# Kernel optimization log

Hardware: AMD Instinct MI355X
Metric: run time of the kernel (lower is better)

## Reference

```python
import jax, jax.numpy as jnp
import numpy as np

DIM = 768
HEADS = 12
HEAD_DIM = DIM // HEADS
HIDDEN = int(DIM * 1.0)  # mlp_ratio = 1.0
EPS = 1e-5


def layer_norm(x, g, b):
    mu = jnp.mean(x, axis=-1, keepdims=True)
    var = jnp.mean(jnp.square(x - mu), axis=-1, keepdims=True)
    return (x - mu) * jax.lax.rsqrt(var + EPS) * g + b


def setup_inputs() -> dict:
    key = jax.random.key(0)
    ks = jax.random.split(key, 8)
    s = 0.02
    return {
        "x": jax.random.normal(ks[0], (8, 1024, DIM), dtype=jnp.float32),
        "mask": jnp.ones((8, 1024), dtype=jnp.int32),
        "g1": jnp.ones((DIM,), jnp.float32),
        "b1": jnp.zeros((DIM,), jnp.float32),
        "w_qkv": jax.random.normal(ks[1], (DIM, 3 * DIM), jnp.float32) * s,
        "w_proj": jax.random.normal(ks[2], (DIM, DIM), jnp.float32) * s,
        "b_proj": jnp.zeros((DIM,), jnp.float32),
        "g2": jnp.ones((DIM,), jnp.float32),
        "b2": jnp.zeros((DIM,), jnp.float32),
        "w_fc1": jax.random.normal(ks[3], (DIM, HIDDEN), jnp.float32) * s,
        "b_fc1": jnp.zeros((HIDDEN,), jnp.float32),
        "w_fc2": jax.random.normal(ks[4], (HIDDEN, DIM), jnp.float32) * s,
        "b_fc2": jnp.zeros((DIM,), jnp.float32),
    }


def reference(x, mask, g1, b1, w_qkv, w_proj, b_proj, g2, b2, w_fc1, b_fc1, w_fc2, b_fc2):
    B, N, C = x.shape
    scale = HEAD_DIM ** -0.5

    # --- attention (pre-norm) ---
    h = layer_norm(x, g1, b1)
    qkv = (h @ w_qkv).reshape(B, N, 3, HEADS, HEAD_DIM)
    qkv = jnp.transpose(qkv, (2, 0, 3, 1, 4))  # 3, b, h, n, d
    q, k, v = qkv[0], qkv[1], qkv[2]

    attn = jnp.einsum("bhnd,bhmd->bhnm", q, k) * scale
    # mask: (B, N) -> pairwise mask (B, 1, N, N)
    pair = (mask[:, None, :, None] * mask[:, None, None, :]) != 0
    attn = jnp.where(pair, attn, jnp.float32(-1e9))
    attn = jax.nn.softmax(attn, axis=-1)

    o = jnp.einsum("bhnm,bhmd->bhnd", attn, v)
    o = jnp.transpose(o, (0, 2, 1, 3)).reshape(B, N, C)
    o = o @ w_proj + b_proj
    x = x + o

    # --- MLP (pre-norm) ---
    h2 = layer_norm(x, g2, b2)
    h2 = jax.nn.gelu(h2 @ w_fc1 + b_fc1, approximate=False)
    h2 = h2 @ w_fc2 + b_fc2
    return x + h2
```

## Files before the change

### kernel.cpp

```cpp
#include <hip/hip_runtime.h>
#include <stdint.h>
#include <math.h>

using short8 = __attribute__((ext_vector_type(8))) short;
using f32x4  = __attribute__((ext_vector_type(4))) float;

#define DEV __device__ __forceinline__
#define S_VMCNT(n) asm volatile("s_waitcnt vmcnt(" #n ")" ::: "memory")
#define S_LGKM(n)  asm volatile("s_waitcnt lgkmcnt(" #n ")" ::: "memory")
#define S_LGKM0()  asm volatile("s_waitcnt lgkmcnt(0)" ::: "memory")
#define SCHED0()   __builtin_amdgcn_sched_barrier(0)
#define SBAR()     __builtin_amdgcn_s_barrier()

DEV unsigned short f2bf(float f) {
    union { float f; unsigned u; } c; c.f = f;
    unsigned u = c.u;
    unsigned r = (u + 0x7FFFu + ((u >> 16) & 1u)) >> 16;
    return (unsigned short)r;
}

DEV float bf2f(unsigned short h) {
    union { unsigned u; float f; } c; c.u = ((unsigned)h) << 16;
    return c.f;
}

DEV void gld16(const unsigned short* g, unsigned short* l) {
    __builtin_amdgcn_global_load_lds(
        (const __attribute__((address_space(1))) void*)g,
        (__attribute__((address_space(3))) void*)l, 16, 0, 0);
}

DEV unsigned ldsaddr(unsigned short* p) {
    return (unsigned)(uintptr_t)(__attribute__((address_space(3))) unsigned short*)p;
}

DEV unsigned cvtpk(float lo, float hi) {
    unsigned r;
    asm("v_cvt_pk_bf16_f32 %0, %1, %2" : "=v"(r) : "v"(lo), "v"(hi));
    return r;
}

DEV uint2 tr16(unsigned addr) {
    uint2 r;
    asm volatile("ds_read_b64_tr_b16 %0, %1" : "=v"(r) : "v"(addr));
    return r;
}

__global__ __launch_bounds__(256) void k_transpose_all(
    const float* __restrict__ w0, const float* __restrict__ w1,
    const float* __restrict__ w2, const float* __restrict__ w3,
    unsigned short* __restrict__ o0, unsigned short* __restrict__ o1,
    unsigned short* __restrict__ o2, unsigned short* __restrict__ o3)
{
    __shared__ float tile[32][33];
    int z = blockIdx.z;
    const float* W = (z == 0) ? w0 : (z == 1) ? w1 : (z == 2) ? w2 : w3;
    unsigned short* Wt = (z == 0) ? o0 : (z == 1) ? o1 : (z == 2) ? o2 : o3;
    int N = (z == 0) ? 2304 : 768;
    int n0 = blockIdx.x * 32, k0 = blockIdx.y * 32;
    if (n0 >= N) return;
    int tx = threadIdx.x, ty = threadIdx.y;
#pragma unroll
    for (int i = 0; i < 4; i++) {
        int k = k0 + ty + i * 8;
        tile[ty + i * 8][tx] = W[(size_t)k * N + n0 + tx];
    }
    __syncthreads();
#pragma unroll
    for (int i = 0; i < 4; i++) {
        int n = n0 + ty + i * 8;
        Wt[(size_t)n * 768 + k0 + tx] = f2bf(tile[tx][ty + i * 8]);
    }
}

template<int BF>
__global__ __launch_bounds__(256) void k_layernorm(
    const void* __restrict__ xin, const float* __restrict__ g,
    const float* __restrict__ b, unsigned short* __restrict__ out)
{
    int row = blockIdx.x;
    int tid = threadIdx.x;
    float v0, v1, v2;
    if (BF) {
        const unsigned short* xr = (const unsigned short*)xin + (size_t)row * 768;
        v0 = bf2f(xr[tid]); v1 = bf2f(xr[tid + 256]); v2 = bf2f(xr[tid + 512]);
    } else {
        const float* xr = (const float*)xin + (size_t)row * 768;
        v0 = xr[tid]; v1 = xr[tid + 256]; v2 = xr[tid + 512];
    }
    float s1 = v0 + v1 + v2;
    float s2 = v0 * v0 + v1 * v1 + v2 * v2;
#pragma unroll
    for (int off = 32; off >= 1; off >>= 1) {
        s1 += __shfl_down(s1, off);
        s2 += __shfl_down(s2, off);
    }
    __shared__ float red[8];
    int wid = tid >> 6, lane = tid & 63;
    if (lane == 0) { red[wid] = s1; red[4 + wid] = s2; }
    __syncthreads();
    s1 = red[0] + red[1] + red[2] + red[3];
    s2 = red[4] + red[5] + red[6] + red[7];
    float mu = s1 * (1.0f / 768.0f);
    float var = s2 * (1.0f / 768.0f) - mu * mu;
    float rs = rsqrtf(var + 1e-5f);
    unsigned short* orow = out + (size_t)row * 768;
    orow[tid]       = f2bf((v0 - mu) * rs * g[tid]       + b[tid]);
    orow[tid + 256] = f2bf((v1 - mu) * rs * g[tid + 256] + b[tid + 256]);
    orow[tid + 512] = f2bf((v2 - mu) * rs * g[tid + 512] + b[tid + 512]);
}

template<int EPI, int BN>
__global__ __launch_bounds__(BN == 128 ? 512 : 256) void k_gemm(
    const unsigned short* __restrict__ A, const unsigned short* __restrict__ Bt,
    const float* __restrict__ bias,
    const float* __restrict__ residF, const unsigned short* __restrict__ residH,
    float* __restrict__ outF, unsigned short* __restrict__ outH,
    unsigned short* __restrict__ qb, unsigned short* __restrict__ kb,
    unsigned short* __restrict__ vtb)
{
    constexpr int KK = 768, NK = 12;
    constexpr int MI = 2;
    constexpr int NJ = 4;
    __shared__ __align__(16) unsigned short As[2][128 * 64];
    __shared__ __align__(16) unsigned short Bs[2][BN * 64];

    int tid = threadIdx.x;
    int lane = tid & 63, wid = tid >> 6;

    int gy = gridDim.y;
    int nwg = 64 * gy;
    int bid = blockIdx.x + blockIdx.y * 64;
    int nid = (bid & 7) * (nwg >> 3) + (bid >> 3);
    int bx = nid / gy;
    int by = nid - bx * gy;
    int m0 = bx * 128, n0 = by * BN;

    int wr = (BN == 128) ? (wid >> 1) * 32 : wid * 32;
    int wc = (BN == 128) ? (wid & 1) * 64 : 0;
    int fr = lane & 15, fg = lane >> 4;
    int fr7 = fr & 7;

    f32x4 zero4 = {0.f, 0.f, 0.f, 0.f};
    f32x4 acc[MI][NJ];
#pragma unroll
    for (int mi = 0; mi < MI; mi++)
#pragma unroll
        for (int nj = 0; nj < NJ; nj++) acc[mi][nj] = zero4;

    int srow = tid >> 3;
    int schk = (tid & 7) ^ ((tid >> 3) & 7);
    const unsigned short* ga = A  + (size_t)(m0 + srow) * KK + schk * 8;
    const unsigned short* gb = Bt + (size_t)(n0 + srow) * KK + schk * 8;

    auto stage = [&](int kt, int s) {
        int ko = kt * 64;
        if constexpr (BN == 128) {
            gld16(ga + ko, As[s] + wid * 512);
            gld16(ga + (size_t)64 * KK + ko, As[s] + 4096 + wid * 512);
            gld16(gb + ko, Bs[s] + wid * 512);
            gld16(gb + (size_t)64 * KK + ko, Bs[s] + 4096 + wid * 512);
        } else {
#pragma unroll
            for (int i = 0; i < 4; i++)
                gld16(ga + (size_t)i * 32 * KK + ko, As[s] + i * 2048 + wid * 512);
#pragma unroll
            for (int i = 0; i < 2; i++)
                gld16(gb + (size_t)i * 32 * KK + ko, Bs[s] + i * 2048 + wid * 512);
        }
    };

    int aoff0 = (wr + fr) * 64;
    int boff0 = (wc + fr) * 64;

    stage(0, 0);

    for (int k = 0; k < NK; ++k) {
        if (k + 1 < NK) {
            stage(k + 1, (k + 1) & 1);
            if constexpr (BN == 128) { S_VMCNT(4); } else { S_VMCNT(6); }
        } else {
            S_VMCNT(0);
        }
        SCHED0(); SBAR(); SCHED0();

        const unsigned short* Ac = As[k & 1];
        const unsigned short* Bc = Bs[k & 1];
#pragma unroll
        for (int kk = 0; kk < 2; ++kk) {
            int off = (((kk << 2) | fg) ^ fr7) * 8;
            short8 af[MI], bfv[NJ];
#pragma unroll
            for (int mi = 0; mi < MI; mi++)
                af[mi] = *(const short8*)(Ac + aoff0 + mi * 1024 + off);
#pragma unroll
            for (int nj = 0; nj < NJ; nj++)
                bfv[nj] = *(const short8*)(Bc + boff0 + nj * 1024 + off);
#pragma unroll
            for (int mi = 0; mi < MI; mi++)
#pragma unroll
                for (int nj = 0; nj < NJ; nj++)
                    acc[mi][nj] = __builtin_amdgcn_mfma_f32_16x16x32_bf16(
                        af[mi], bfv[nj], acc[mi][nj], 0, 0, 0);
        }
        SCHED0(); SBAR(); SCHED0();
    }

#pragma unroll
    for (int mi = 0; mi < MI; mi++) {
#pragma unroll
        for (int nj = 0; nj < NJ; nj++) {
#pragma unroll
            for (int i = 0; i < 4; i++) {
                int grow = m0 + wr + mi * 16 + fg * 4 + i;
                int gcol = n0 + wc + nj * 16 + fr;
                float v = acc[mi][nj][i];
                if (EPI == 0) {
                    int part = gcol / 768;
                    int wi = gcol - part * 768;
                    int head = wi >> 6, d = wi & 63;
                    int bb = grow >> 10, n = grow & 1023;
                    size_t base = ((size_t)(bb * 12 + head)) << 16;
                    unsigned short bv = f2bf(v);
                    if (part == 0)      qb[base + (size_t)n * 64 + d] = bv;
                    else if (part == 1) kb[base + (size_t)n * 64 + d] = bv;
                    else                vtb[base + (size_t)d * 1024 + n] = bv;
                } else if (EPI == 1) {
                    size_t idx = (size_t)grow * 768 + gcol;
                    outH[idx] = f2bf(v + bias[gcol] + residF[idx]);
                } else if (EPI == 2) {
                    float t = v + bias[gcol];
                    outH[(size_t)grow * 768 + gcol] =
                        f2bf(0.5f * t * (1.0f + erff(t * 0.70710678118f)));
                } else {
                    size_t idx = (size_t)grow * 768 + gcol;
                    outF[idx] = v + bias[gcol] + bf2f(residH[idx]);
                }
            }
        }
    }
}

__global__ __launch_bounds__(512) void k_attn(
    const unsigned short* __restrict__ Q, const unsigned short* __restrict__ Kk,
    const unsigned short* __restrict__ Vt, const int* __restrict__ mask,
    unsigned short* __restrict__ O)
{
    __shared__ __align__(16) unsigned short KsA[3 * 4096];
    __shared__ __align__(16) unsigned short VsA[3 * 4096];
    __shared__ __align__(16) unsigned short PT[8 * 1024];
    __shared__ float mskf[1024];

    int tid = threadIdx.x, lane = tid & 63, wid = tid >> 6;
    int bid = blockIdx.x + blockIdx.y * 8;
    int nid = (bid & 7) * 96 + (bid >> 3);
    int qt = nid & 7;
    int bh = nid >> 3;
    int b = bh / 12;
    int hh = bh - b * 12;
    int fr = lane & 15, fg = lane >> 4;

    const unsigned short* qg = Q  + ((size_t)bh << 16);
    const unsigned short* kg = Kk + ((size_t)bh << 16);
    const unsigned short* vg = Vt + ((size_t)bh << 16);

    for (int i = tid; i < 1024; i += 512)
        mskf[i] = mask[b * 1024 + i] ? 1.f : 0.f;

    short8 qf[2];
    {
        const unsigned short* qp = qg + (size_t)(qt * 128 + wid * 16 + fr) * 64 + fg * 8;
        qf[0] = *(const short8*)(qp);
        qf[1] = *(const short8*)(qp + 32);
    }

    int srow = wid * 8 + (lane >> 3);
    int schk = (lane & 7) ^ ((lane >> 3) & 7);
    const unsigned short* kgp = kg + (size_t)srow * 64 + schk * 8;
    const unsigned short* vgp = vg + (size_t)srow * 1024 + schk * 8;

    auto stage = [&](int kn, int s) {
        gld16(kgp + (size_t)(kn * 64) * 64, &KsA[s * 4096] + wid * 512);
        gld16(vgp + kn * 64, &VsA[s * 4096] + wid * 512);
    };

    stage(0, 0);
    __syncthreads();

    f32x4 zero4 = {0.f, 0.f, 0.f, 0.f};
    f32x4 oacc[4];
    f32x4 lacc = zero4;
#pragma unroll
    for (int df = 0; df < 4; df++) oacc[df] = zero4;

    short8 ones8;
#pragma unroll
    for (int j = 0; j < 8; j++) ones8[j] = (short)0x3F80;

    const float SC = 0.125f * 1.44269504f;

    unsigned short* pw = &PT[wid * 1024];
    unsigned trbase = ldsaddr(pw) + fg * 256 + fr * 2;

    int pos0 = fg ^ (fr & 7);
    int pos1 = (fg + 4) ^ (fr & 7);

#pragma unroll
    for (int kc = 0; kc < 16; ++kc) {
        S_VMCNT(0);
        SCHED0(); SBAR(); SCHED0();
        if (kc < 15) { stage(kc + 1, (kc + 1) % 3); SCHED0(); }

        const unsigned short* Kc = &KsA[(kc % 3) * 4096];
        short8 kb0[4], kb1[4];
#pragma unroll
        for (int nf = 0; nf < 4; ++nf) {
            int row = nf * 16 + fr;
            kb0[nf] = *(const short8*)(Kc + row * 64 + pos0 * 8);
            kb1[nf] = *(const short8*)(Kc + row * 64 + pos1 * 8);
        }
        SCHED0();

        f32x4 s[4];
        if (kc > 0) {
            S_LGKM(8);
            uint2 r00 = tr16(trbase);
            uint2 r01 = tr16(trbase + 128);
            uint2 r10 = tr16(trbase + 1024);
            uint2 r11 = tr16(trbase + 1024 + 128);
            S_LGKM(4);
            SCHED0();
            __builtin_amdgcn_s_setprio(1);
#pragma unroll
            for (int nf = 0; nf < 4; ++nf) {
                f32x4 a = zero4;
                a = __builtin_amdgcn_mfma_f32_16x16x32_bf16(qf[0], kb0[nf], a, 0, 0, 0);
                a = __builtin_amdgcn_mfma_f32_16x16x32_bf16(qf[1], kb1[nf], a, 0, 0, 0);
                s[nf] = a;
            }
            __builtin_amdgcn_s_setprio(0);

            const unsigned short* Vp = &VsA[(((kc - 1) % 3)) * 4096];
            short8 vb0[4], vb1[4];
#pragma unroll
            for (int df = 0; df < 4; ++df) {
                int rv = df * 16 + fr;
                vb0[df] = *(const short8*)(Vp + rv * 64 + pos0 * 8);
                vb1[df] = *(const short8*)(Vp + rv * 64 + pos1 * 8);
            }

            union { unsigned u[4]; short8 s8; } pa0, pa1;
            pa0.u[0] = r00.x; pa0.u[1] = r00.y; pa0.u[2] = r01.x; pa0.u[3] = r01.y;
            pa1.u[0] = r10.x; pa1.u[1] = r10.y; pa1.u[2] = r11.x; pa1.u[3] = r11.y;

            uint2 w[4];
#pragma unroll
            for (int nf = 0; nf < 4; nf++) {
                float mk = mskf[kc * 64 + nf * 16 + fr];
                float p0 = __builtin_amdgcn_exp2f(s[nf][0] * SC) * mk;
                float p1 = __builtin_amdgcn_exp2f(s[nf][1] * SC) * mk;
                float p2 = __builtin_amdgcn_exp2f(s[nf][2] * SC) * mk;
                float p3 = __builtin_amdgcn_exp2f(s[nf][3] * SC) * mk;
                w[nf].x = cvtpk(p0, p1); w[nf].y = cvtpk(p2, p3);
            }

            S_LGKM0();
            SCHED0();
            __builtin_amdgcn_s_setprio(1);
#pragma unroll
            for (int df = 0; df < 4; df++) {
                oacc[df] = __builtin_amdgcn_mfma_f32_16x16x32_bf16(pa0.s8, vb0[df], oacc[df], 0, 0, 0);
                oacc[df] = __builtin_amdgcn_mfma_f32_16x16x32_bf16(pa1.s8, vb1[df], oacc[df], 0, 0, 0);
            }
            lacc = __builtin_amdgcn_mfma_f32_16x16x32_bf16(pa0.s8, ones8, lacc, 0, 0, 0);
            lacc = __builtin_amdgcn_mfma_f32_16x16x32_bf16(pa1.s8, ones8, lacc, 0, 0, 0);
            __builtin_amdgcn_s_setprio(0);

#pragma unroll
            for (int nf = 0; nf < 4; nf++)
                *(uint2*)(pw + (nf * 16 + fr) * 16 + fg * 4) = w[nf];
        } else {
            S_LGKM0();
            SCHED0();
            __builtin_amdgcn_s_setprio(1);
#pragma unroll
            for (int nf = 0; nf < 4; ++nf) {
                f32x4 a = zero4;
                a = __builtin_amdgcn_mfma_f32_16x16x32_bf16(qf[0], kb0[nf], a, 0, 0, 0);
                a = __builtin_amdgcn_mfma_f32_16x16x32_bf16(qf[1], kb1[nf], a, 0, 0, 0);
                s[nf] = a;
            }
            __builtin_amdgcn_s_setprio(0);
#pragma unroll
            for (int nf = 0; nf < 4; nf++) {
                float mk = mskf[nf * 16 + fr];
                float p0 = __builtin_amdgcn_exp2f(s[nf][0] * SC) * mk;
                float p1 = __builtin_amdgcn_exp2f(s[nf][1] * SC) * mk;
                float p2 = __builtin_amdgcn_exp2f(s[nf][2] * SC) * mk;
                float p3 = __builtin_amdgcn_exp2f(s[nf][3] * SC) * mk;
                uint2 w0; w0.x = cvtpk(p0, p1); w0.y = cvtpk(p2, p3);
                *(uint2*)(pw + (nf * 16 + fr) * 16 + fg * 4) = w0;
            }
        }
    }

    {
        uint2 r00 = tr16(trbase);
        uint2 r01 = tr16(trbase + 128);
        uint2 r10 = tr16(trbase + 1024);
        uint2 r11 = tr16(trbase + 1024 + 128);
        const unsigned short* Vp = &VsA[0];
        short8 vb0[4], vb1[4];
#pragma unroll
        for (int df = 0; df < 4; ++df) {
            int rv = df * 16 + fr;
            vb0[df] = *(const short8*)(Vp + rv * 64 + pos0 * 8);
            vb1[df] = *(const short8*)(Vp + rv * 64 + pos1 * 8);
        }
        S_LGKM0(); SCHED0();
        union { unsigned u[4]; short8 s8; } pa0, pa1;
        pa0.u[0] = r00.x; pa0.u[1] = r00.y; pa0.u[2] = r01.x; pa0.u[3] = r01.y;
        pa1.u[0] = r10.x; pa1.u[1] = r10.y; pa1.u[2] = r11.x; pa1.u[3] = r11.y;
#pragma unroll
        for (int df = 0; df < 4; df++) {
            oacc[df] = __builtin_amdgcn_mfma_f32_16x16x32_bf16(pa0.s8, vb0[df], oacc[df], 0, 0, 0);
            oacc[df] = __builtin_amdgcn_mfma_f32_16x16x32_bf16(pa1.s8, vb1[df], oacc[df], 0, 0, 0);
        }
        lacc = __builtin_amdgcn_mfma_f32_16x16x32_bf16(pa0.s8, ones8, lacc, 0, 0, 0);
        lacc = __builtin_amdgcn_mfma_f32_16x16x32_bf16(pa1.s8, ones8, lacc, 0, 0, 0);
    }

#pragma unroll
    for (int i = 0; i < 4; i++) {
        float inv = 1.0f / fmaxf(lacc[i], 1e-30f);
        size_t rowbase = ((size_t)(b * 1024 + qt * 128 + wid * 16 + fg * 4 + i)) * 768
                         + hh * 64 + fr;
#pragma unroll
        for (int df = 0; df < 4; df++)
            O[rowbase + df * 16] = f2bf(oacc[df][i] * inv);
    }
}

extern "C" void kernel_launch(void* const* d_in, const int* in_sizes, int n_in,
                              void* d_out, int out_size, void* d_ws, size_t ws_size,
                              hipStream_t stream)
{
    const float* x      = (const float*)d_in[0];
    const int*   mask   = (const int*)d_in[1];
    const float* g1     = (const float*)d_in[2];
    const float* b1     = (const float*)d_in[3];
    const float* w_qkv  = (const float*)d_in[4];
    const float* w_proj = (const float*)d_in[5];
    const float* b_proj = (const float*)d_in[6];
    const float* g2     = (const float*)d_in[7];
    const float* b2     = (const float*)d_in[8];
    const float* w_fc1  = (const float*)d_in[9];
    const float* b_fc1  = (const float*)d_in[10];
    const float* w_fc2  = (const float*)d_in[11];
    const float* b_fc2  = (const float*)d_in[12];
    float* out = (float*)d_out;

    char* ws = (char*)d_ws;
    unsigned short* wqkv_t  = (unsigned short*)(ws + 0);
    unsigned short* wproj_t = (unsigned short*)(ws + 3538944);
    unsigned short* wfc1_t  = (unsigned short*)(ws + 4718592);
    unsigned short* wfc2_t  = (unsigned short*)(ws + 5898240);
    unsigned short* bufA    = (unsigned short*)(ws + 7077888);
    unsigned short* bufB    = (unsigned short*)(ws + 19660800);
    unsigned short* qb      = (unsigned short*)(ws + 32243712);
    unsigned short* kb      = (unsigned short*)(ws + 44826624);
    unsigned short* vtb     = (unsigned short*)(ws + 57409536);
    unsigned short* x1b     = (unsigned short*)(ws + 69992448);

    k_transpose_all<<<dim3(72, 24, 4), dim3(32, 8), 0, stream>>>(
        w_qkv, w_proj, w_fc1, w_fc2, wqkv_t, wproj_t, wfc1_t, wfc2_t);

    k_layernorm<0><<<8192, 256, 0, stream>>>(x, g1, b1, bufA);

    k_gemm<0, 128><<<dim3(64, 18), 512, 0, stream>>>(bufA, wqkv_t,
        nullptr, nullptr, nullptr, nullptr, nullptr, qb, kb, vtb);

    k_attn<<<dim3(8, 96), 512, 0, stream>>>(qb, kb, vtb, mask, bufB);

    k_gemm<1, 64><<<dim3(64, 12), 256, 0, stream>>>(bufB, wproj_t,
        b_proj, x, nullptr, nullptr, x1b, nullptr, nullptr, nullptr);

    k_layernorm<1><<<8192, 256, 0, stream>>>(x1b, g2, b2, bufA);

    k_gemm<2, 64><<<dim3(64, 12), 256, 0, stream>>>(bufA, wfc1_t,
        b_fc1, nullptr, nullptr, nullptr, bufB, nullptr, nullptr, nullptr);

    k_gemm<3, 64><<<dim3(64, 12), 256, 0, stream>>>(bufB, wfc2_t,
        b_fc2, nullptr, x1b, out, nullptr, nullptr, nullptr, nullptr);
}
```

Measured before the change: 176.8 us.

## Load GEMM A-operand directly into registers instead of staging through LDS

```diff
diff --git a/kernel.cpp b/kernel.cpp
--- a/kernel.cpp
+++ b/kernel.cpp
@@ -110,8 +110,8 @@
     orow[tid + 512] = f2bf((v2 - mu) * rs * g[tid + 512] + b[tid + 512]);
 }
 
-template<int EPI, int BN>
-__global__ __launch_bounds__(BN == 128 ? 512 : 256) void k_gemm(
+template<int EPI, int BN, int NT>
+__global__ __launch_bounds__(NT) void k_gemm(
     const unsigned short* __restrict__ A, const unsigned short* __restrict__ Bt,
     const float* __restrict__ bias,
     const float* __restrict__ residF, const unsigned short* __restrict__ residH,
@@ -120,9 +120,7 @@
     unsigned short* __restrict__ vtb)
 {
     constexpr int KK = 768, NK = 12;
-    constexpr int MI = 2;
-    constexpr int NJ = 4;
-    __shared__ __align__(16) unsigned short As[2][128 * 64];
+    constexpr int MI = 2, NJ = 4;
     __shared__ __align__(16) unsigned short Bs[2][BN * 64];
 
     int tid = threadIdx.x;
@@ -148,51 +146,60 @@
 #pragma unroll
         for (int nj = 0; nj < NJ; nj++) acc[mi][nj] = zero4;
 
+    const unsigned short* aptr = A + (size_t)(m0 + wr + fr) * KK + fg * 8;
+
     int srow = tid >> 3;
-    int schk = (tid & 7) ^ ((tid >> 3) & 7);
-    const unsigned short* ga = A  + (size_t)(m0 + srow) * KK + schk * 8;
+    int schk = (tid & 7) ^ (srow & 7);
     const unsigned short* gb = Bt + (size_t)(n0 + srow) * KK + schk * 8;
 
-    auto stage = [&](int kt, int s) {
+    auto stageB = [&](int kt, int s) {
         int ko = kt * 64;
         if constexpr (BN == 128) {
-            gld16(ga + ko, As[s] + wid * 512);
-            gld16(ga + (size_t)64 * KK + ko, As[s] + 4096 + wid * 512);
             gld16(gb + ko, Bs[s] + wid * 512);
             gld16(gb + (size_t)64 * KK + ko, Bs[s] + 4096 + wid * 512);
         } else {
-#pragma unroll
-            for (int i = 0; i < 4; i++)
-                gld16(ga + (size_t)i * 32 * KK + ko, As[s] + i * 2048 + wid * 512);
-#pragma unroll
-            for (int i = 0; i < 2; i++)
-                gld16(gb + (size_t)i * 32 * KK + ko, Bs[s] + i * 2048 + wid * 512);
+            gld16(gb + ko, Bs[s] + wid * 512);
+            gld16(gb + (size_t)32 * KK + ko, Bs[s] + 2048 + wid * 512);
         }
     };
 
-    int aoff0 = (wr + fr) * 64;
+    short8 ar[2][MI][2];
+
+    stageB(0, 0);
+    SCHED0();
+#pragma unroll
+    for (int mi = 0; mi < MI; mi++)
+#pragma unroll
+        for (int kk = 0; kk < 2; kk++)
+            ar[0][mi][kk] = *(const short8*)(aptr + (size_t)mi * 16 * KK + kk * 32);
+    SCHED0();
+
     int boff0 = (wc + fr) * 64;
 
-    stage(0, 0);
-
+#pragma unroll
     for (int k = 0; k < NK; ++k) {
         if (k + 1 < NK) {
-            stage(k + 1, (k + 1) & 1);
-            if constexpr (BN == 128) { S_VMCNT(4); } else { S_VMCNT(6); }
+            stageB(k + 1, (k + 1) & 1);
+            SCHED0();
+            int ko = (k + 1) * 64;
+#pragma unroll
+            for (int mi = 0; mi < MI; mi++)
+#pragma unroll
+                for (int kk = 0; kk < 2; kk++)
+                    ar[(k + 1) & 1][mi][kk] =
+                        *(const short8*)(aptr + (size_t)mi * 16 * KK + ko + kk * 32);
+            SCHED0();
+            S_VMCNT(6);
         } else {
             S_VMCNT(0);
         }
         SCHED0(); SBAR(); SCHED0();
 
-        const unsigned short* Ac = As[k & 1];
         const unsigned short* Bc = Bs[k & 1];
 #pragma unroll
         for (int kk = 0; kk < 2; ++kk) {
             int off = (((kk << 2) | fg) ^ fr7) * 8;
-            short8 af[MI], bfv[NJ];
-#pragma unroll
-            for (int mi = 0; mi < MI; mi++)
-                af[mi] = *(const short8*)(Ac + aoff0 + mi * 1024 + off);
+            short8 bfv[NJ];
 #pragma unroll
             for (int nj = 0; nj < NJ; nj++)
                 bfv[nj] = *(const short8*)(Bc + boff0 + nj * 1024 + off);
@@ -201,7 +208,7 @@
 #pragma unroll
                 for (int nj = 0; nj < NJ; nj++)
                     acc[mi][nj] = __builtin_amdgcn_mfma_f32_16x16x32_bf16(
-                        af[mi], bfv[nj], acc[mi][nj], 0, 0, 0);
+                        ar[k & 1][mi][kk], bfv[nj], acc[mi][nj], 0, 0, 0);
         }
         SCHED0(); SBAR(); SCHED0();
     }
@@ -477,19 +484,19 @@
 
     k_layernorm<0><<<8192, 256, 0, stream>>>(x, g1, b1, bufA);
 
-    k_gemm<0, 128><<<dim3(64, 18), 512, 0, stream>>>(bufA, wqkv_t,
+    k_gemm<0, 128, 512><<<dim3(64, 18), 512, 0, stream>>>(bufA, wqkv_t,
         nullptr, nullptr, nullptr, nullptr, nullptr, qb, kb, vtb);
 
     k_attn<<<dim3(8, 96), 512, 0, stream>>>(qb, kb, vtb, mask, bufB);
 
-    k_gemm<1, 64><<<dim3(64, 12), 256, 0, stream>>>(bufB, wproj_t,
+    k_gemm<1, 64, 256><<<dim3(64, 12), 256, 0, stream>>>(bufB, wproj_t,
         b_proj, x, nullptr, nullptr, x1b, nullptr, nullptr, nullptr);
 
     k_layernorm<1><<<8192, 256, 0, stream>>>(x1b, g2, b2, bufA);
 
-    k_gemm<2, 64><<<dim3(64, 12), 256, 0, stream>>>(bufA, wfc1_t,
+    k_gemm<2, 64, 256><<<dim3(64, 12), 256, 0, stream>>>(bufA, wfc1_t,
         b_fc1, nullptr, nullptr, nullptr, bufB, nullptr, nullptr, nullptr);
 
-    k_gemm<3, 64><<<dim3(64, 12), 256, 0, stream>>>(bufB, wfc2_t,
+    k_gemm<3, 64, 256><<<dim3(64, 12), 256, 0, stream>>>(bufB, wfc2_t,
         b_fc2, nullptr, x1b, out, nullptr, nullptr, nullptr, nullptr);
 }
```

Result: slower. 229.6 us (+29.9%).

## Fuse LN1 with weight transpose, stage V transpose via LDS, use bf16 residual

Applied to the files above, without the earlier changes.

```diff
diff --git a/kernel.cpp b/kernel.cpp
--- a/kernel.cpp
+++ b/kernel.cpp
@@ -46,48 +46,84 @@
     return r;
 }
 
-__global__ __launch_bounds__(256) void k_transpose_all(
+__global__ __launch_bounds__(256) void k_prep(
+    const float* __restrict__ x, const float* __restrict__ g,
+    const float* __restrict__ b, unsigned short* __restrict__ h_out,
+    unsigned short* __restrict__ xb,
     const float* __restrict__ w0, const float* __restrict__ w1,
     const float* __restrict__ w2, const float* __restrict__ w3,
     unsigned short* __restrict__ o0, unsigned short* __restrict__ o1,
     unsigned short* __restrict__ o2, unsigned short* __restrict__ o3)
 {
     __shared__ float tile[32][33];
-    int z = blockIdx.z;
-    const float* W = (z == 0) ? w0 : (z == 1) ? w1 : (z == 2) ? w2 : w3;
-    unsigned short* Wt = (z == 0) ? o0 : (z == 1) ? o1 : (z == 2) ? o2 : o3;
-    int N = (z == 0) ? 2304 : 768;
-    int n0 = blockIdx.x * 32, k0 = blockIdx.y * 32;
-    if (n0 >= N) return;
-    int tx = threadIdx.x, ty = threadIdx.y;
-#pragma unroll
-    for (int i = 0; i < 4; i++) {
-        int k = k0 + ty + i * 8;
-        tile[ty + i * 8][tx] = W[(size_t)k * N + n0 + tx];
-    }
-    __syncthreads();
-#pragma unroll
-    for (int i = 0; i < 4; i++) {
-        int n = n0 + ty + i * 8;
-        Wt[(size_t)n * 768 + k0 + tx] = f2bf(tile[tx][ty + i * 8]);
-    }
-}
-
-template<int BF>
-__global__ __launch_bounds__(256) void k_layernorm(
-    const void* __restrict__ xin, const float* __restrict__ g,
+    __shared__ float red[8];
+    int bid = blockIdx.x;
+    int tid = threadIdx.x;
+
+    if (bid < 8192) {
+        int row = bid;
+        const float* xr = x + (size_t)row * 768;
+        float v0 = xr[tid], v1 = xr[tid + 256], v2 = xr[tid + 512];
+        float s1 = v0 + v1 + v2;
+        float s2 = v0 * v0 + v1 * v1 + v2 * v2;
+#pragma unroll
+        for (int off = 32; off >= 1; off >>= 1) {
+            s1 += __shfl_down(s1, off);
+            s2 += __shfl_down(s2, off);
+        }
+        int wid = tid >> 6, lane = tid & 63;
+        if (lane == 0) { red[wid] = s1; red[4 + wid] = s2; }
+        __syncthreads();
+        s1 = red[0] + red[1] + red[2] + red[3];
+        s2 = red[4] + red[5] + red[6] + red[7];
+        float mu = s1 * (1.0f / 768.0f);
+        float var = s2 * (1.0f / 768.0f) - mu * mu;
+        float rs = rsqrtf(var + 1e-5f);
+        unsigned short* orow = h_out + (size_t)row * 768;
+        unsigned short* xrow = xb + (size_t)row * 768;
+        orow[tid]       = f2bf((v0 - mu) * rs * g[tid]       + b[tid]);
+        orow[tid + 256] = f2bf((v1 - mu) * rs * g[tid + 256] + b[tid + 256]);
+        orow[tid + 512] = f2bf((v2 - mu) * rs * g[tid + 512] + b[tid + 512]);
+        xrow[tid]       = f2bf(v0);
+        xrow[tid + 256] = f2bf(v1);
+        xrow[tid + 512] = f2bf(v2);
+    } else {
+        int idx = bid - 8192;
+        const float* W; unsigned short* Wt; int N, n0, k0;
+        if (idx < 1728) {
+            W = w0; Wt = o0; N = 2304;
+            n0 = (idx % 72) * 32; k0 = (idx / 72) * 32;
+        } else {
+            idx -= 1728;
+            int z = idx / 576, r = idx % 576;
+            W = (z == 0) ? w1 : (z == 1) ? w2 : w3;
+            Wt = (z == 0) ? o1 : (z == 1) ? o2 : o3;
+            N = 768;
+            n0 = (r % 24) * 32; k0 = (r / 24) * 32;
+        }
+        int tx = tid & 31, ty = tid >> 5;
+#pragma unroll
+        for (int i = 0; i < 4; i++) {
+            int k = k0 + ty + i * 8;
+            tile[ty + i * 8][tx] = W[(size_t)k * N + n0 + tx];
+        }
+        __syncthreads();
+#pragma unroll
+        for (int i = 0; i < 4; i++) {
+            int n = n0 + ty + i * 8;
+            Wt[(size_t)n * 768 + k0 + tx] = f2bf(tile[tx][ty + i * 8]);
+        }
+    }
+}
+
+__global__ __launch_bounds__(256) void k_layernorm_bf(
+    const unsigned short* __restrict__ xin, const float* __restrict__ g,
     const float* __restrict__ b, unsigned short* __restrict__ out)
 {
     int row = blockIdx.x;
     int tid = threadIdx.x;
-    float v0, v1, v2;
-    if (BF) {
-        const unsigned short* xr = (const unsigned short*)xin + (size_t)row * 768;
-        v0 = bf2f(xr[tid]); v1 = bf2f(xr[tid + 256]); v2 = bf2f(xr[tid + 512]);
-    } else {
-        const float* xr = (const float*)xin + (size_t)row * 768;
-        v0 = xr[tid]; v1 = xr[tid + 256]; v2 = xr[tid + 512];
-    }
+    const unsigned short* xr = xin + (size_t)row * 768;
+    float v0 = bf2f(xr[tid]), v1 = bf2f(xr[tid + 256]), v2 = bf2f(xr[tid + 512]);
     float s1 = v0 + v1 + v2;
     float s2 = v0 * v0 + v1 * v1 + v2 * v2;
 #pragma unroll
@@ -113,8 +149,7 @@
 template<int EPI, int BN>
 __global__ __launch_bounds__(BN == 128 ? 512 : 256) void k_gemm(
     const unsigned short* __restrict__ A, const unsigned short* __restrict__ Bt,
-    const float* __restrict__ bias,
-    const float* __restrict__ residF, const unsigned short* __restrict__ residH,
+    const float* __restrict__ bias, const unsigned short* __restrict__ residH,
     float* __restrict__ outF, unsigned short* __restrict__ outH,
     unsigned short* __restrict__ qb, unsigned short* __restrict__ kb,
     unsigned short* __restrict__ vtb)
@@ -204,6 +239,38 @@
                         af[mi], bfv[nj], acc[mi][nj], 0, 0, 0);
         }
         SCHED0(); SBAR(); SCHED0();
+    }
+
+    if (EPI == 0 && n0 >= 1536) {
+        unsigned short* Ct = &As[0][0];
+#pragma unroll
+        for (int mi = 0; mi < MI; mi++) {
+#pragma unroll
+            for (int nj = 0; nj < NJ; nj++) {
+                int row = wc + nj * 16 + fr;
+                int colb = wr + mi * 16 + fg * 4;
+                int ch = (colb >> 3) ^ (row & 15);
+                uint2 w;
+                w.x = cvtpk(acc[mi][nj][0], acc[mi][nj][1]);
+                w.y = cvtpk(acc[mi][nj][2], acc[mi][nj][3]);
+                *(uint2*)(Ct + row * 128 + ch * 8 + (colb & 7)) = w;
+            }
+        }
+        __syncthreads();
+        int r = tid >> 2;
+        int h0 = (n0 - 1536) >> 6;
+        int bb = m0 >> 10;
+        int nbase = m0 & 1023;
+        size_t vbase = ((size_t)(bb * 12 + h0 + (r >> 6)) << 16)
+                     + (size_t)(r & 63) * 1024 + nbase;
+#pragma unroll
+        for (int j = 0; j < 4; j++) {
+            int c = (tid & 3) * 4 + j;
+            int ch = c ^ (r & 15);
+            uint4 v4 = *(const uint4*)(Ct + r * 128 + ch * 8);
+            *(uint4*)(vtb + vbase + c * 8) = v4;
+        }
+        return;
     }
 
 #pragma unroll
@@ -222,12 +289,11 @@
                     int bb = grow >> 10, n = grow & 1023;
                     size_t base = ((size_t)(bb * 12 + head)) << 16;
                     unsigned short bv = f2bf(v);
-                    if (part == 0)      qb[base + (size_t)n * 64 + d] = bv;
-                    else if (part == 1) kb[base + (size_t)n * 64 + d] = bv;
-                    else                vtb[base + (size_t)d * 1024 + n] = bv;
+                    if (part == 0) qb[base + (size_t)n * 64 + d] = bv;
+                    else           kb[base + (size_t)n * 64 + d] = bv;
                 } else if (EPI == 1) {
                     size_t idx = (size_t)grow * 768 + gcol;
-                    outH[idx] = f2bf(v + bias[gcol] + residF[idx]);
+                    outH[idx] = f2bf(v + bias[gcol] + bf2f(residH[idx]));
                 } else if (EPI == 2) {
                     float t = v + bias[gcol];
                     outH[(size_t)grow * 768 + gcol] =
@@ -471,25 +537,24 @@
     unsigned short* kb      = (unsigned short*)(ws + 44826624);
     unsigned short* vtb     = (unsigned short*)(ws + 57409536);
     unsigned short* x1b     = (unsigned short*)(ws + 69992448);
-
-    k_transpose_all<<<dim3(72, 24, 4), dim3(32, 8), 0, stream>>>(
+    unsigned short* xb      = (unsigned short*)(ws + 82575360);
+
+    k_prep<<<8192 + 3456, 256, 0, stream>>>(x, g1, b1, bufA, xb,
         w_qkv, w_proj, w_fc1, w_fc2, wqkv_t, wproj_t, wfc1_t, wfc2_t);
 
-    k_layernorm<0><<<8192, 256, 0, stream>>>(x, g1, b1, bufA);
-
     k_gemm<0, 128><<<dim3(64, 18), 512, 0, stream>>>(bufA, wqkv_t,
-        nullptr, nullptr, nullptr, nullptr, nullptr, qb, kb, vtb);
+        nullptr, nullptr, nullptr, nullptr, qb, kb, vtb);
 
     k_attn<<<dim3(8, 96), 512, 0, stream>>>(qb, kb, vtb, mask, bufB);
 
     k_gemm<1, 64><<<dim3(64, 12), 256, 0, stream>>>(bufB, wproj_t,
-        b_proj, x, nullptr, nullptr, x1b, nullptr, nullptr, nullptr);
-
-    k_layernorm<1><<<8192, 256, 0, stream>>>(x1b, g2, b2, bufA);
+        b_proj, xb, nullptr, x1b, nullptr, nullptr, nullptr);
+
+    k_layernorm_bf<<<8192, 256, 0, stream>>>(x1b, g2, b2, bufA);
 
     k_gemm<2, 64><<<dim3(64, 12), 256, 0, stream>>>(bufA, wfc1_t,
-        b_fc1, nullptr, nullptr, nullptr, bufB, nullptr, nullptr, nullptr);
+        b_fc1, nullptr, nullptr, bufB, nullptr, nullptr, nullptr);
 
     k_gemm<3, 64><<<dim3(64, 12), 256, 0, stream>>>(bufB, wfc2_t,
-        b_fc2, nullptr, x1b, out, nullptr, nullptr, nullptr, nullptr);
-}
+        b_fc2, x1b, out, nullptr, nullptr, nullptr, nullptr);
+}
```

Result: faster. 158.9 us (-10.1%).
